# Performance work log

Measured on AMD Instinct MI355X. Metric: run time of the kernel, lower is better.

Reference implementation:

```python
import jax, jax.numpy as jnp
import numpy as np

MASK_THR = 0.005   # cfg.mask_thr
SIGMA = 2.0        # cfg.sigma (gaussian kernel)
N, G, H, W = 500, 128, 200, 304


def setup_inputs() -> dict:
    key = jax.random.key(0)
    k1, k2, k3, k4, k5, k6 = jax.random.split(key, 6)
    return {
        "cate_scores": jax.random.uniform(k1, (N,), jnp.float32),
        "seg_preds_x": jax.random.uniform(k2, (G, H, W), jnp.float32),
        "seg_preds_y": jax.random.uniform(k3, (G, H, W), jnp.float32),
        "cate_labels": jax.random.randint(k4, (N,), 0, 80),
        "x_inds": jax.random.randint(k5, (N,), 0, G),
        "y_inds": jax.random.randint(k6, (N,), 0, G),
    }


def reference(cate_scores, seg_preds_x, seg_preds_y, cate_labels, x_inds, y_inds):
    # --- SOLO decoupled mask decoding: irregular grid-index gather ---
    mask_x = seg_preds_x[x_inds]                 # [N,H,W]
    mask_y = seg_preds_y[y_inds]                 # [N,H,W]
    soft = mask_x * mask_y                       # seg_masks_soft
    hard = (soft > MASK_THR).astype(soft.dtype)  # seg_masks (binary)
    sum_masks = hard.sum((1, 2))                 # [N] mask areas
    # mask-quality rescoring
    seg_score = (soft * hard).sum((1, 2)) / jnp.maximum(sum_masks, 1.0)
    scores = cate_scores * seg_score

    # --- Matrix NMS (gaussian kernel) ---
    flat = hard.reshape(N, -1)                   # [N, H*W]
    inter = flat @ flat.T                        # [N,N] intersection areas
    union = sum_masks[:, None] + sum_masks[None, :] - inter
    iou = jnp.triu(inter / jnp.maximum(union, 1e-6), k=1)
    label_eq = jnp.triu((cate_labels[:, None] == cate_labels[None, :]).astype(soft.dtype), k=1)
    decay_iou = iou * label_eq                   # same-class IoU, upper tri
    comp_iou = decay_iou.max(0)                  # [N] max IoU with higher-scored same-class mask
    decay_matrix = jnp.exp(-SIGMA * decay_iou ** 2)
    comp_matrix = jnp.exp(-SIGMA * comp_iou ** 2)[:, None]  # expand(n,n).T in torch
    decay_coef = (decay_matrix / comp_matrix).min(0)         # [N]
    return scores * decay_coef
```

## Files before the change

### kernel.cpp

```cpp
#include <hip/hip_runtime.h>


#define N_DET 500
#define HW    (200 * 304)
#define TILE  64
#define NT    (HW / TILE)
#define PSTR  512
#define LSTR  65
#define MASK_THR 0.005f
#define SIGMA 2.0f

__global__ __launch_bounds__(512) void maskgen_kernel(
    const float* __restrict__ seg_x, const float* __restrict__ seg_y,
    const int* __restrict__ x_inds, const int* __restrict__ y_inds,
    unsigned long long* __restrict__ packed_t,
    float* __restrict__ part_sum)
{
    __shared__ float sx[128 * LSTR];
    __shared__ float sy[128 * LSTR];
    const int t   = blockIdx.x;
    const int tid = threadIdx.x;
    const int base = t * TILE;

    for (int e = tid; e < 128 * 16; e += 512) {
        const int r  = e >> 4;
        const int c4 = (e & 15) << 2;
        const float4 vx = *(const float4*)(seg_x + (size_t)r * HW + base + c4);
        const float4 vy = *(const float4*)(seg_y + (size_t)r * HW + base + c4);
        float* dx = sx + r * LSTR + c4;
        float* dy = sy + r * LSTR + c4;
        dx[0] = vx.x; dx[1] = vx.y; dx[2] = vx.z; dx[3] = vx.w;
        dy[0] = vy.x; dy[1] = vy.y; dy[2] = vy.z; dy[3] = vy.w;
    }
    __syncthreads();

    if (tid < N_DET) {
        const float* __restrict__ rx = sx + x_inds[tid] * LSTR;
        const float* __restrict__ ry = sy + y_inds[tid] * LSTR;
        float ssum = 0.0f;
        unsigned int lo = 0u, hi = 0u;
        #pragma unroll
        for (int p = 0; p < 32; ++p) {
            const float v = rx[p] * ry[p];
            if (v > MASK_THR) { ssum += v; lo |= (1u << p); }
        }
        #pragma unroll
        for (int p = 0; p < 32; ++p) {
            const float v = rx[32 + p] * ry[32 + p];
            if (v > MASK_THR) { ssum += v; hi |= (1u << p); }
        }
        packed_t[(size_t)t * PSTR + tid] = ((unsigned long long)hi << 32) | lo;
        part_sum[(size_t)t * PSTR + tid] = ssum;
    }
}

__global__ __launch_bounds__(256) void pair_iou_kernel(
    const unsigned long long* __restrict__ packed_t,
    const float* __restrict__ part_sum,
    const int* __restrict__ labels,
    const float* __restrict__ cate_scores,
    float* __restrict__ d2col,
    float* __restrict__ comp2,
    float* __restrict__ scores)
{
    const int j   = blockIdx.x;
    const int tid = threadIdx.x;
    const int lane = tid & 63, wav = tid >> 6;

    __shared__ int   s_lab[N_DET];
    __shared__ int   s_list[N_DET];
    __shared__ int   s_cnt;
    __shared__ float s_red[4];
    __shared__ float s_max[4];

    if (tid == 0) s_cnt = 0;
    for (int i = tid; i < N_DET; i += 256) {
        s_lab[i] = labels[i];
        d2col[(size_t)j * N_DET + i] = 0.0f;
    }
    __syncthreads();

    const int lj = s_lab[j];
    for (int i = tid; i < j; i += 256)
        if (s_lab[i] == lj) { const int p = atomicAdd(&s_cnt, 1); s_list[p] = i; }

    unsigned long long bj[15];
    float cj_part = 0.0f;
    #pragma unroll
    for (int q = 0; q < 15; ++q) {
        const int w = lane + (q << 6);
        bj[q] = (w < NT) ? packed_t[(size_t)w * PSTR + j] : 0ull;
        cj_part += (float)__popcll(bj[q]);
    }
    #pragma unroll
    for (int off = 32; off; off >>= 1) cj_part += __shfl_down(cj_part, off);
    const float cj = __shfl(cj_part, 0);

    float S = 0.0f;
    for (int t = tid; t < NT; t += 256) S += part_sum[(size_t)t * PSTR + j];
    #pragma unroll
    for (int off = 32; off; off >>= 1) S += __shfl_down(S, off);
    if (lane == 0) s_red[wav] = S;
    __syncthreads();
    if (tid == 0) {
        const float Sj = s_red[0] + s_red[1] + s_red[2] + s_red[3];
        scores[j] = cate_scores[j] * (Sj / fmaxf(cj, 1.0f));
    }
    const int cnt = s_cnt;

    float wmax = 0.0f;
    for (int p = wav; p < cnt; p += 4) {
        const int i = s_list[p];
        int inter = 0, ci = 0;
        #pragma unroll
        for (int q = 0; q < 15; ++q) {
            const int w = lane + (q << 6);
            if (w < NT) {
                const unsigned long long a = packed_t[(size_t)w * PSTR + i];
                inter += __popcll(a & bj[q]);
                ci    += __popcll(a);
            }
        }
        #pragma unroll
        for (int off = 32; off; off >>= 1) {
            inter += __shfl_down(inter, off);
            ci    += __shfl_down(ci,    off);
        }
        if (lane == 0) {
            const float uni = (float)ci + cj - (float)inter;
            const float iou = (float)inter / fmaxf(uni, 1e-6f);
            d2col[(size_t)j * N_DET + i] = iou * iou;
            wmax = fmaxf(wmax, iou);
        }
    }
    if (lane == 0) s_max[wav] = wmax;
    __syncthreads();
    if (tid == 0) {
        const float c = fmaxf(fmaxf(s_max[0], s_max[1]), fmaxf(s_max[2], s_max[3]));
        comp2[j] = c * c;
    }
}

__global__ __launch_bounds__(64) void decay_kernel(
    const float* __restrict__ d2col,
    const float* __restrict__ comp2,
    const float* __restrict__ scores,
    float* __restrict__ out)
{
    const int j = blockIdx.x;
    const int lane = threadIdx.x;
    float m = 1e30f;
    for (int i = lane; i < N_DET; i += 64)
        m = fminf(m, comp2[i] - d2col[(size_t)j * N_DET + i]);
    #pragma unroll
    for (int off = 32; off; off >>= 1)
        m = fminf(m, __shfl_down(m, off));
    if (lane == 0) out[j] = scores[j] * expf(SIGMA * m);
}

extern "C" void kernel_launch(void* const* d_in, const int* in_sizes, int n_in,
                              void* d_out, int out_size, void* d_ws, size_t ws_size,
                              hipStream_t stream) {
    const float* cate_scores = (const float*)d_in[0];
    const float* seg_x       = (const float*)d_in[1];
    const float* seg_y       = (const float*)d_in[2];
    const int*   labels      = (const int*)d_in[3];
    const int*   x_inds      = (const int*)d_in[4];
    const int*   y_inds      = (const int*)d_in[5];
    float* out = (float*)d_out;

    char* ws = (char*)d_ws;
    unsigned long long* packed_t = (unsigned long long*)(ws + 0);
    float* part_sum = (float*)(ws + 3891200);
    float* d2col    = (float*)(ws + 5836800);
    float* scores   = (float*)(ws + 6836800);
    float* comp2    = (float*)(ws + 6838800);

    maskgen_kernel <<<NT, 512, 0, stream>>>(seg_x, seg_y, x_inds, y_inds,
                                            packed_t, part_sum);
    pair_iou_kernel<<<N_DET, 256, 0, stream>>>(packed_t, part_sum, labels,
                                               cate_scores, d2col, comp2, scores);
    decay_kernel   <<<N_DET, 64, 0, stream>>>(d2col, comp2, scores, out);
}
```

Measured before the change: 136.0 us.

## Transpose packed mask bits to detection-major layout and vectorize shared loads

Adds a transpose kernel that rewrites the tile-major packed bitmasks and partial sums into detection-major rows. The pair IoU kernel can then read each detection's bits contiguously with 128-bit loads instead of strided 8-byte gathers. The maskgen kernel also pads its shared rows to 68 floats and uses float4 for both shared stores and loads. The cost is an extra launch and an extra round trip through global memory for the transposed data.

```diff
diff --git a/kernel.cpp b/kernel.cpp
--- a/kernel.cpp
+++ b/kernel.cpp
@@ -6,7 +6,9 @@
 #define TILE  64
 #define NT    (HW / TILE)
 #define PSTR  512
-#define LSTR  65
+#define DSTR  950
+#define NW2   (NT / 2)
+#define LSTR  68
 #define MASK_THR 0.005f
 #define SIGMA 2.0f
 
@@ -16,8 +18,8 @@
     unsigned long long* __restrict__ packed_t,
     float* __restrict__ part_sum)
 {
-    __shared__ float sx[128 * LSTR];
-    __shared__ float sy[128 * LSTR];
+    __shared__ __align__(16) float sx[128 * LSTR];
+    __shared__ __align__(16) float sy[128 * LSTR];
     const int t   = blockIdx.x;
     const int tid = threadIdx.x;
     const int base = t * TILE;
@@ -25,12 +27,8 @@
     for (int e = tid; e < 128 * 16; e += 512) {
         const int r  = e >> 4;
         const int c4 = (e & 15) << 2;
-        const float4 vx = *(const float4*)(seg_x + (size_t)r * HW + base + c4);
-        const float4 vy = *(const float4*)(seg_y + (size_t)r * HW + base + c4);
-        float* dx = sx + r * LSTR + c4;
-        float* dy = sy + r * LSTR + c4;
-        dx[0] = vx.x; dx[1] = vx.y; dx[2] = vx.z; dx[3] = vx.w;
-        dy[0] = vy.x; dy[1] = vy.y; dy[2] = vy.z; dy[3] = vy.w;
+        *(float4*)(sx + r * LSTR + c4) = *(const float4*)(seg_x + (size_t)r * HW + base + c4);
+        *(float4*)(sy + r * LSTR + c4) = *(const float4*)(seg_y + (size_t)r * HW + base + c4);
     }
     __syncthreads();
 
@@ -40,23 +38,73 @@
         float ssum = 0.0f;
         unsigned int lo = 0u, hi = 0u;
         #pragma unroll
-        for (int p = 0; p < 32; ++p) {
-            const float v = rx[p] * ry[p];
-            if (v > MASK_THR) { ssum += v; lo |= (1u << p); }
-        }
-        #pragma unroll
-        for (int p = 0; p < 32; ++p) {
-            const float v = rx[32 + p] * ry[32 + p];
-            if (v > MASK_THR) { ssum += v; hi |= (1u << p); }
+        for (int k = 0; k < 8; ++k) {
+            const float4 xv = *(const float4*)(rx + (k << 2));
+            const float4 yv = *(const float4*)(ry + (k << 2));
+            const float p0 = xv.x * yv.x, p1 = xv.y * yv.y,
+                        p2 = xv.z * yv.z, p3 = xv.w * yv.w;
+            if (p0 > MASK_THR) { ssum += p0; lo |= 1u << (4 * k); }
+            if (p1 > MASK_THR) { ssum += p1; lo |= 1u << (4 * k + 1); }
+            if (p2 > MASK_THR) { ssum += p2; lo |= 1u << (4 * k + 2); }
+            if (p3 > MASK_THR) { ssum += p3; lo |= 1u << (4 * k + 3); }
+        }
+        #pragma unroll
+        for (int k = 0; k < 8; ++k) {
+            const float4 xv = *(const float4*)(rx + 32 + (k << 2));
+            const float4 yv = *(const float4*)(ry + 32 + (k << 2));
+            const float p0 = xv.x * yv.x, p1 = xv.y * yv.y,
+                        p2 = xv.z * yv.z, p3 = xv.w * yv.w;
+            if (p0 > MASK_THR) { ssum += p0; hi |= 1u << (4 * k); }
+            if (p1 > MASK_THR) { ssum += p1; hi |= 1u << (4 * k + 1); }
+            if (p2 > MASK_THR) { ssum += p2; hi |= 1u << (4 * k + 2); }
+            if (p3 > MASK_THR) { ssum += p3; hi |= 1u << (4 * k + 3); }
         }
         packed_t[(size_t)t * PSTR + tid] = ((unsigned long long)hi << 32) | lo;
         part_sum[(size_t)t * PSTR + tid] = ssum;
     }
 }
 
-__global__ __launch_bounds__(256) void pair_iou_kernel(
+__global__ __launch_bounds__(256) void transpose_kernel(
     const unsigned long long* __restrict__ packed_t,
     const float* __restrict__ part_sum,
+    unsigned long long* __restrict__ packed_d,
+    float* __restrict__ part_sumT)
+{
+    __shared__ unsigned long long tp[64 * 65];
+    __shared__ float              ts[64 * 65];
+    const int t0  = blockIdx.x * 64;
+    const int d0  = blockIdx.y * 64;
+    const int tid = threadIdx.x;
+    const int lane = tid & 63, wav = tid >> 6;
+
+    #pragma unroll
+    for (int k = 0; k < 16; ++k) {
+        const int r  = (k << 2) + wav;
+        const int gt = t0 + r;
+        unsigned long long v = 0ull; float s = 0.0f;
+        if (gt < NT) {
+            v = packed_t[(size_t)gt * PSTR + d0 + lane];
+            s = part_sum[(size_t)gt * PSTR + d0 + lane];
+        }
+        tp[r * 65 + lane] = v;
+        ts[r * 65 + lane] = s;
+    }
+    __syncthreads();
+    const int gt = t0 + lane;
+    #pragma unroll
+    for (int k = 0; k < 16; ++k) {
+        const int m = (k << 2) + wav;
+        const int d = d0 + m;
+        if (gt < NT && d < N_DET) {
+            packed_d [(size_t)d * DSTR + gt] = tp[lane * 65 + m];
+            part_sumT[(size_t)d * DSTR + gt] = ts[lane * 65 + m];
+        }
+    }
+}
+
+__global__ __launch_bounds__(256) void pair_iou_kernel(
+    const unsigned long long* __restrict__ packed_d,
+    const float* __restrict__ part_sumT,
     const int* __restrict__ labels,
     const float* __restrict__ cate_scores,
     float* __restrict__ d2col,
@@ -84,20 +132,23 @@
     for (int i = tid; i < j; i += 256)
         if (s_lab[i] == lj) { const int p = atomicAdd(&s_cnt, 1); s_list[p] = i; }
 
-    unsigned long long bj[15];
+    const ulonglong2* __restrict__ pj2 = (const ulonglong2*)(packed_d + (size_t)j * DSTR);
+    ulonglong2 bj[8];
     float cj_part = 0.0f;
     #pragma unroll
-    for (int q = 0; q < 15; ++q) {
+    for (int q = 0; q < 8; ++q) {
         const int w = lane + (q << 6);
-        bj[q] = (w < NT) ? packed_t[(size_t)w * PSTR + j] : 0ull;
-        cj_part += (float)__popcll(bj[q]);
+        if (w < NW2) {
+            bj[q] = pj2[w];
+            cj_part += (float)(__popcll(bj[q].x) + __popcll(bj[q].y));
+        } else { bj[q].x = 0ull; bj[q].y = 0ull; }
     }
     #pragma unroll
     for (int off = 32; off; off >>= 1) cj_part += __shfl_down(cj_part, off);
     const float cj = __shfl(cj_part, 0);
 
     float S = 0.0f;
-    for (int t = tid; t < NT; t += 256) S += part_sum[(size_t)t * PSTR + j];
+    for (int t = tid; t < NT; t += 256) S += part_sumT[(size_t)j * DSTR + t];
     #pragma unroll
     for (int off = 32; off; off >>= 1) S += __shfl_down(S, off);
     if (lane == 0) s_red[wav] = S;
@@ -111,14 +162,15 @@
     float wmax = 0.0f;
     for (int p = wav; p < cnt; p += 4) {
         const int i = s_list[p];
+        const ulonglong2* __restrict__ pi2 = (const ulonglong2*)(packed_d + (size_t)i * DSTR);
         int inter = 0, ci = 0;
         #pragma unroll
-        for (int q = 0; q < 15; ++q) {
+        for (int q = 0; q < 8; ++q) {
             const int w = lane + (q << 6);
-            if (w < NT) {
-                const unsigned long long a = packed_t[(size_t)w * PSTR + i];
-                inter += __popcll(a & bj[q]);
-                ci    += __popcll(a);
+            if (w < NW2) {
+                const ulonglong2 a = pi2[w];
+                inter += __popcll(a.x & bj[q].x) + __popcll(a.y & bj[q].y);
+                ci    += __popcll(a.x) + __popcll(a.y);
             }
         }
         #pragma unroll
@@ -171,14 +223,18 @@
 
     char* ws = (char*)d_ws;
     unsigned long long* packed_t = (unsigned long long*)(ws + 0);
-    float* part_sum = (float*)(ws + 3891200);
-    float* d2col    = (float*)(ws + 5836800);
-    float* scores   = (float*)(ws + 6836800);
-    float* comp2    = (float*)(ws + 6838800);
-
-    maskgen_kernel <<<NT, 512, 0, stream>>>(seg_x, seg_y, x_inds, y_inds,
-                                            packed_t, part_sum);
-    pair_iou_kernel<<<N_DET, 256, 0, stream>>>(packed_t, part_sum, labels,
-                                               cate_scores, d2col, comp2, scores);
-    decay_kernel   <<<N_DET, 64, 0, stream>>>(d2col, comp2, scores, out);
-}
+    float* part_sum  = (float*)(ws + 3891200);
+    unsigned long long* packed_d = (unsigned long long*)(ws + 5836800);
+    float* part_sumT = (float*)(ws + 9636800);
+    float* d2col     = (float*)(ws + 11536800);
+    float* scores    = (float*)(ws + 12536800);
+    float* comp2     = (float*)(ws + 12538800);
+
+    maskgen_kernel  <<<NT, 512, 0, stream>>>(seg_x, seg_y, x_inds, y_inds,
+                                             packed_t, part_sum);
+    transpose_kernel<<<dim3(15, 8), 256, 0, stream>>>(packed_t, part_sum,
+                                                      packed_d, part_sumT);
+    pair_iou_kernel <<<N_DET, 256, 0, stream>>>(packed_d, part_sumT, labels,
+                                                cate_scores, d2col, comp2, scores);
+    decay_kernel    <<<N_DET, 64, 0, stream>>>(d2col, comp2, scores, out);
+}
```

Measured after the change: 130.6 us. -4.0%, faster.
